# Performance work log

Hardware: AMD Instinct MI355X
Metric: run time of the kernel (lower is better)

## Reference

```python
import jax, jax.numpy as jnp
import numpy as np

B = 128          # batch of codewords
M_CHK = 288      # n_check_nodes
N_VAR = 576      # n_variable_nodes
K_INFO = 288     # n_information_bits
N_ITER = 5
EDGE_P = 0.02    # ~11-12 edges per check row, LDPC-like sparsity


def setup_inputs() -> dict:
    key = jax.random.key(0)
    k1, k2, k3, k4 = jax.random.split(key, 4)
    inputs = jax.random.normal(k1, (B, N_VAR), dtype=jnp.float32)
    # sparse binary parity-check matrix, batched (keras RNN constants carry batch dim)
    H = jax.random.bernoulli(k2, EDGE_P, (B, M_CHK, N_VAR)).astype(jnp.float32)
    sigma2 = 0.5 + 0.5 * jax.random.uniform(k3, (B, 1), dtype=jnp.float32)
    # learned parameters
    input_ponderation = jnp.ones((N_ITER, 1), dtype=jnp.float32)
    out_ponderation = jnp.ones((N_ITER, 1), dtype=jnp.float32)
    skip_ponderation = jnp.ones((1, 1), dtype=jnp.float32)
    # per-edge check-to-variable weights of the neural BP cell
    w_cv = 1.0 + 0.02 * jax.random.normal(k4, (M_CHK, N_VAR), dtype=jnp.float32)
    gate_logit = jnp.asarray(0.0, dtype=jnp.float32)
    return {"inputs": inputs, "H": H, "sigma2": sigma2,
            "input_ponderation": input_ponderation,
            "out_ponderation": out_ponderation,
            "skip_ponderation": skip_ponderation,
            "w_cv": w_cv, "gate_logit": gate_logit}


def _decode(inputs, H, sigma2, input_ponderation, out_ponderation,
            skip_ponderation, w_cv, gate_logit):
    llrs = -4.0 * inputs / sigma2                                    # [B, n]
    # trainable=True path: normalize by mean |llr|
    norm_llrs = llrs / jnp.mean(jnp.abs(llrs), axis=-1, keepdims=True)
    # tile over iterations and apply input ponderation -> [B, T, n]
    x = norm_llrs[:, None, :] * input_ponderation

    mask = H                                                         # [B, m, n]
    gate = jax.nn.sigmoid(gate_logit)

    def cell(Mstate, x_t):
        # variable-to-check extrinsic messages on edges
        S = jnp.sum(Mstate, axis=1, keepdims=True)                   # [B, 1, n]
        V = (x_t[:, None, :] + S - Mstate) * mask                    # [B, m, n]
        # tanh-product check-node update (product excluding self via divide)
        t = jnp.tanh(0.5 * jnp.clip(V, -15.0, 15.0))
        t_edge = jnp.where(mask > 0, t, 1.0)
        P = jnp.prod(t_edge, axis=-1, keepdims=True)                 # [B, m, 1]
        t_safe = jnp.where(jnp.abs(t_edge) < 1e-7,
                           jnp.where(t_edge >= 0, 1e-7, -1e-7), t_edge)
        r = jnp.clip(P / t_safe, -1.0 + 1e-6, 1.0 - 1e-6)
        M_new = 2.0 * jnp.arctanh(r) * w_cv * mask                   # weighted c2v
        # gated (damped) state update
        M_out = gate * M_new + (1.0 - gate) * Mstate
        posterior = x_t + jnp.sum(M_out, axis=1)                     # [B, n]
        return M_out, posterior

    M0 = jnp.zeros_like(H)
    xs = jnp.swapaxes(x, 0, 1)                                       # [T, B, n]
    _, posts = jax.lax.scan(cell, M0, xs)
    outputs = jnp.swapaxes(posts, 0, 1)                              # [B, T, n]

    # post-normalization per iteration, weighted pooling over iterations
    norm_out = outputs / jnp.mean(jnp.abs(outputs), axis=-1, keepdims=True)
    pooled = jnp.mean(out_ponderation * norm_out, axis=-2)           # [B, n]
    out = pooled + skip_ponderation * norm_llrs                      # [1,1] broadcast
    return jax.nn.sigmoid(-out[:, :K_INFO])


def reference(inputs, H, sigma2, input_ponderation, out_ponderation,
              skip_ponderation, w_cv, gate_logit):
    return _decode(inputs, H, sigma2, input_ponderation, out_ponderation,
                   skip_ponderation, w_cv, gate_logit)
```

## Files before the change

### kernel.cpp

```cpp
#include <hip/hip_runtime.h>

#define B_SZ 128
#define MCHK 288
#define NVAR 576
#define KINFO 288
#define NITER 5
#define CAP 40
#define LCAP 3712
#define TPB 1024

__global__ __launch_bounds__(TPB) void decode(
    const float* __restrict__ inp,   const float* __restrict__ H,
    const float* __restrict__ sigma2,
    const float* __restrict__ ipond, const float* __restrict__ opond,
    const float* __restrict__ skipp, const float* __restrict__ wcv,
    const float* __restrict__ gatel, float* __restrict__ out) {

    __shared__ __align__(16) float MT[2 * LCAP];
    __shared__ unsigned int ev[LCAP];
    __shared__ float xln[NVAR];
    __shared__ float S[NVAR];
    __shared__ float pooled[NVAR];
    __shared__ float Prow[MCHK];
    __shared__ int   rcnt[MCHK];
    __shared__ int   roff[MCHK];
    __shared__ float red[16];
    __shared__ int   wsumI[16];
    __shared__ float scal;
    __shared__ int   EtotS;

    float* const Mld = MT;
    float* const tld = MT + LCAP;
    unsigned short* const stage = (unsigned short*)MT;

    const int b    = blockIdx.x;
    const int tid  = threadIdx.x;
    const int wid  = tid >> 6;
    const int lane = tid & 63;

    const float sig  = sigma2[b];
    const float gate = 1.0f / (1.0f + __expf(-gatel[0]));
    const float gbar = 1.0f - gate;
    const float skip = skipp[0];

    float l = 0.0f;
    if (tid < NVAR) l = -4.0f * inp[(size_t)b * NVAR + tid] / sig;

    const float* Hb = H + (size_t)b * (MCHK * NVAR);
    for (int m = wid; m < MCHK; m += 16) {
        const float* hrow = Hb + (size_t)m * NVAR;
        const float4* h4  = (const float4*)hrow;
        float4 a  = h4[lane];
        float4 bq = h4[64 + lane];
        float  c  = hrow[512 + lane];
        int cnt = (a.x!=0.f)+(a.y!=0.f)+(a.z!=0.f)+(a.w!=0.f)
                + (bq.x!=0.f)+(bq.y!=0.f)+(bq.z!=0.f)+(bq.w!=0.f) + (c!=0.f);
        int pre = cnt;
        #pragma unroll
        for (int o = 1; o < 64; o <<= 1) {
            int n = __shfl_up(pre, o, 64);
            if (lane >= o) pre += n;
        }
        int p = pre - cnt;
        unsigned short* dst = stage + m * CAP;
        int base = lane * 4;
        if (a.x!=0.f)  { if (p<CAP) dst[p] = (unsigned short)(base    ); p++; }
        if (a.y!=0.f)  { if (p<CAP) dst[p] = (unsigned short)(base + 1); p++; }
        if (a.z!=0.f)  { if (p<CAP) dst[p] = (unsigned short)(base + 2); p++; }
        if (a.w!=0.f)  { if (p<CAP) dst[p] = (unsigned short)(base + 3); p++; }
        if (bq.x!=0.f) { if (p<CAP) dst[p] = (unsigned short)(256 + base    ); p++; }
        if (bq.y!=0.f) { if (p<CAP) dst[p] = (unsigned short)(256 + base + 1); p++; }
        if (bq.z!=0.f) { if (p<CAP) dst[p] = (unsigned short)(256 + base + 2); p++; }
        if (bq.w!=0.f) { if (p<CAP) dst[p] = (unsigned short)(256 + base + 3); p++; }
        if (c!=0.f)    { if (p<CAP) dst[p] = (unsigned short)(512 + lane);     p++; }
        if (lane == 63) rcnt[m] = (pre > CAP) ? CAP : pre;
    }
    __syncthreads();

    int myc = 0, incl = 0;
    if (tid < 320) {
        myc  = (tid < MCHK) ? rcnt[tid] : 0;
        incl = myc;
        #pragma unroll
        for (int o = 1; o < 64; o <<= 1) {
            int n = __shfl_up(incl, o, 64);
            if (lane >= o) incl += n;
        }
        if (lane == 63) wsumI[wid] = incl;
    }
    __syncthreads();
    if (tid < MCHK) {
        int o = incl - myc;
        #pragma unroll
        for (int w = 0; w < 4; ++w) if (w < wid) o += wsumI[w];
        int c = myc;
        if (o >= LCAP)         { o = 0; c = 0; }
        else if (o + c > LCAP) { c = LCAP - o; }
        roff[tid] = o; rcnt[tid] = c;
        const unsigned short* sg = stage + tid * CAP;
        for (int j = 0; j < c; ++j)
            ev[o + j] = ((unsigned)tid << 16) | (unsigned)sg[j];
    }
    if (tid == 0) {
        int e = wsumI[0] + wsumI[1] + wsumI[2] + wsumI[3] + wsumI[4];
        EtotS = (e > LCAP) ? LCAP : e;
    }
    __syncthreads();
    const int E = EtotS;

    float al = (tid < NVAR) ? fabsf(l) : 0.0f;
    #pragma unroll
    for (int o = 32; o; o >>= 1) al += __shfl_down(al, o, 64);
    if (lane == 0) red[wid] = al;
    for (int e = tid; e < E; e += TPB) Mld[e] = 0.0f;
    if (tid < NVAR) { S[tid] = 0.0f; pooled[tid] = 0.0f; }
    __syncthreads();
    if (tid == 0) {
        float s = 0.0f;
        #pragma unroll
        for (int i = 0; i < 16; ++i) s += red[i];
        scal = (float)NVAR / s;
    }
    __syncthreads();
    if (tid < NVAR) xln[tid] = l * scal;
    __syncthreads();

    float ipl[NITER], opl[NITER];
    #pragma unroll
    for (int t = 0; t < NITER; ++t) { ipl[t] = ipond[t]; opl[t] = opond[t]; }

    for (int t = 0; t < NITER; ++t) {
        const float pt = ipl[t], ot = opl[t];

        for (int e = tid; e < E; e += TPB) {
            int v   = (int)(ev[e] & 0xFFFFu);
            float V = fmaf(pt, xln[v], S[v]) - Mld[e];
            V = fminf(15.0f, fmaxf(-15.0f, V));
            float ex = __expf(V);
            float te = (ex - 1.0f) * __builtin_amdgcn_rcpf(ex + 1.0f);
            float x  = 0.5f * V, x2 = x * x;
            float tp = x * fmaf(x2, fmaf(x2, fmaf(x2, -0.05396825f, 0.13333333f),
                                         -0.33333333f), 1.0f);
            tld[e] = (fabsf(V) < 0.5f) ? tp : te;
        }
        __syncthreads();

        if (tid < MCHK) {
            int c = rcnt[tid], o = roff[tid];
            float P = 1.0f;
            for (int j = 0; j < c; ++j) P *= tld[o + j];
            Prow[tid] = P;
        }
        if (tid < NVAR) S[tid] = 0.0f;
        __syncthreads();

        for (int e = tid; e < E; e += TPB) {
            unsigned pk = ev[e];
            int v = (int)(pk & 0xFFFFu);
            int m = (int)(pk >> 16);
            float tj = tld[e];
            float ts = (fabsf(tj) < 1e-7f) ? ((tj >= 0.0f) ? 1e-7f : -1e-7f) : tj;
            float r  = Prow[m] * __builtin_amdgcn_rcpf(ts);
            r = fminf(1.0f - 1e-6f, fmaxf(-1.0f + 1e-6f, r));
            float w  = wcv[m * NVAR + v];
            float Mn = __logf((1.0f + r) * __builtin_amdgcn_rcpf(1.0f - r)) * w;
            float Mo = fmaf(gate, Mn, gbar * Mld[e]);
            Mld[e] = Mo;
            atomicAdd(&S[v], Mo);
        }
        __syncthreads();

        float post = 0.0f, ap = 0.0f;
        if (tid < NVAR) { post = fmaf(pt, xln[tid], S[tid]); ap = fabsf(post); }
        #pragma unroll
        for (int o = 32; o; o >>= 1) ap += __shfl_down(ap, o, 64);
        if (lane == 0) red[wid] = ap;
        __syncthreads();
        if (tid == 0) {
            float s2 = 0.0f;
            #pragma unroll
            for (int i = 0; i < 16; ++i) s2 += red[i];
            scal = (float)NVAR / s2;
        }
        __syncthreads();
        if (tid < NVAR) pooled[tid] += ot * post * scal;
    }

    if (tid < KINFO) {
        float o = pooled[tid] * (1.0f / NITER) + skip * xln[tid];
        out[(size_t)b * KINFO + tid] = 1.0f / (1.0f + __expf(o));
    }
}

extern "C" void kernel_launch(void* const* d_in, const int* in_sizes, int n_in,
                              void* d_out, int out_size, void* d_ws, size_t ws_size,
                              hipStream_t stream) {
    const float* inp    = (const float*)d_in[0];
    const float* H      = (const float*)d_in[1];
    const float* sigma2 = (const float*)d_in[2];
    const float* ipond  = (const float*)d_in[3];
    const float* opond  = (const float*)d_in[4];
    const float* skipp  = (const float*)d_in[5];
    const float* wcv    = (const float*)d_in[6];
    const float* gatel  = (const float*)d_in[7];
    float* out = (float*)d_out;

    decode<<<B_SZ, TPB, 0, stream>>>(inp, H, sigma2, ipond, opond, skipp,
                                     wcv, gatel, out);
}
```

Baseline: 177.2 us.

## Keep per-edge state in registers, prefetch H rows, drop serial reduction syncs

Per-edge messages, edge indices, edge weights and tanh values now live in registers (up to 4 edges per thread) rather than in LDS, and the w_cv gather is hoisted out of the iteration loop. H row loads are software-prefetched one row-group ahead during edge-list construction. The single-thread scale reductions with their extra barriers are replaced by every thread summing the 16 partials redundantly. This shrinks LDS use and cuts barriers and global gathers, at the cost of more registers and a hard cap of 4096 edges per block, which LCAP already enforces.

```diff
diff --git a/kernel.cpp b/kernel.cpp
--- a/kernel.cpp
+++ b/kernel.cpp
@@ -8,6 +8,7 @@
 #define CAP 40
 #define LCAP 3712
 #define TPB 1024
+#define EPT 4
 
 __global__ __launch_bounds__(TPB) void decode(
     const float* __restrict__ inp,   const float* __restrict__ H,
@@ -16,7 +17,7 @@
     const float* __restrict__ skipp, const float* __restrict__ wcv,
     const float* __restrict__ gatel, float* __restrict__ out) {
 
-    __shared__ __align__(16) float MT[2 * LCAP];
+    __shared__ __align__(16) float MT[(MCHK * CAP) / 2];
     __shared__ unsigned int ev[LCAP];
     __shared__ float xln[NVAR];
     __shared__ float S[NVAR];
@@ -26,11 +27,9 @@
     __shared__ int   roff[MCHK];
     __shared__ float red[16];
     __shared__ int   wsumI[16];
-    __shared__ float scal;
     __shared__ int   EtotS;
 
-    float* const Mld = MT;
-    float* const tld = MT + LCAP;
+    float* const tld = MT;
     unsigned short* const stage = (unsigned short*)MT;
 
     const int b    = blockIdx.x;
@@ -43,37 +42,55 @@
     const float gbar = 1.0f - gate;
     const float skip = skipp[0];
 
+    float ipl[NITER], opl[NITER];
+    #pragma unroll
+    for (int t = 0; t < NITER; ++t) { ipl[t] = ipond[t]; opl[t] = opond[t]; }
+
     float l = 0.0f;
     if (tid < NVAR) l = -4.0f * inp[(size_t)b * NVAR + tid] / sig;
-
-    const float* Hb = H + (size_t)b * (MCHK * NVAR);
-    for (int m = wid; m < MCHK; m += 16) {
-        const float* hrow = Hb + (size_t)m * NVAR;
-        const float4* h4  = (const float4*)hrow;
-        float4 a  = h4[lane];
-        float4 bq = h4[64 + lane];
-        float  c  = hrow[512 + lane];
-        int cnt = (a.x!=0.f)+(a.y!=0.f)+(a.z!=0.f)+(a.w!=0.f)
-                + (bq.x!=0.f)+(bq.y!=0.f)+(bq.z!=0.f)+(bq.w!=0.f) + (c!=0.f);
-        int pre = cnt;
-        #pragma unroll
-        for (int o = 1; o < 64; o <<= 1) {
-            int n = __shfl_up(pre, o, 64);
-            if (lane >= o) pre += n;
-        }
-        int p = pre - cnt;
-        unsigned short* dst = stage + m * CAP;
-        int base = lane * 4;
-        if (a.x!=0.f)  { if (p<CAP) dst[p] = (unsigned short)(base    ); p++; }
-        if (a.y!=0.f)  { if (p<CAP) dst[p] = (unsigned short)(base + 1); p++; }
-        if (a.z!=0.f)  { if (p<CAP) dst[p] = (unsigned short)(base + 2); p++; }
-        if (a.w!=0.f)  { if (p<CAP) dst[p] = (unsigned short)(base + 3); p++; }
-        if (bq.x!=0.f) { if (p<CAP) dst[p] = (unsigned short)(256 + base    ); p++; }
-        if (bq.y!=0.f) { if (p<CAP) dst[p] = (unsigned short)(256 + base + 1); p++; }
-        if (bq.z!=0.f) { if (p<CAP) dst[p] = (unsigned short)(256 + base + 2); p++; }
-        if (bq.w!=0.f) { if (p<CAP) dst[p] = (unsigned short)(256 + base + 3); p++; }
-        if (c!=0.f)    { if (p<CAP) dst[p] = (unsigned short)(512 + lane);     p++; }
-        if (lane == 63) rcnt[m] = (pre > CAP) ? CAP : pre;
+    float al = (tid < NVAR) ? fabsf(l) : 0.0f;
+    #pragma unroll
+    for (int o = 32; o; o >>= 1) al += __shfl_down(al, o, 64);
+    if (lane == 0) red[wid] = al;
+
+    {
+        const float* Hb = H + (size_t)b * (MCHK * NVAR);
+        const float* hr0 = Hb + (size_t)wid * NVAR;
+        float4 a  = ((const float4*)hr0)[lane];
+        float4 bq = ((const float4*)hr0)[64 + lane];
+        float  hc = hr0[512 + lane];
+        for (int m = wid; m < MCHK; m += 16) {
+            const int mn = m + 16;
+            float4 na = a, nbq = bq; float nhc = hc;
+            if (mn < MCHK) {
+                const float* hr = Hb + (size_t)mn * NVAR;
+                na  = ((const float4*)hr)[lane];
+                nbq = ((const float4*)hr)[64 + lane];
+                nhc = hr[512 + lane];
+            }
+            int cnt = (a.x!=0.f)+(a.y!=0.f)+(a.z!=0.f)+(a.w!=0.f)
+                    + (bq.x!=0.f)+(bq.y!=0.f)+(bq.z!=0.f)+(bq.w!=0.f) + (hc!=0.f);
+            int pre = cnt;
+            #pragma unroll
+            for (int o = 1; o < 64; o <<= 1) {
+                int n = __shfl_up(pre, o, 64);
+                if (lane >= o) pre += n;
+            }
+            int p = pre - cnt;
+            unsigned short* dst = stage + m * CAP;
+            int base = lane * 4;
+            if (a.x!=0.f)  { if (p<CAP) dst[p] = (unsigned short)(base    ); p++; }
+            if (a.y!=0.f)  { if (p<CAP) dst[p] = (unsigned short)(base + 1); p++; }
+            if (a.z!=0.f)  { if (p<CAP) dst[p] = (unsigned short)(base + 2); p++; }
+            if (a.w!=0.f)  { if (p<CAP) dst[p] = (unsigned short)(base + 3); p++; }
+            if (bq.x!=0.f) { if (p<CAP) dst[p] = (unsigned short)(256 + base    ); p++; }
+            if (bq.y!=0.f) { if (p<CAP) dst[p] = (unsigned short)(256 + base + 1); p++; }
+            if (bq.z!=0.f) { if (p<CAP) dst[p] = (unsigned short)(256 + base + 2); p++; }
+            if (bq.w!=0.f) { if (p<CAP) dst[p] = (unsigned short)(256 + base + 3); p++; }
+            if (hc!=0.f)   { if (p<CAP) dst[p] = (unsigned short)(512 + lane);     p++; }
+            if (lane == 63) rcnt[m] = (pre > CAP) ? CAP : pre;
+            a = na; bq = nbq; hc = nhc;
+        }
     }
     __syncthreads();
 
@@ -101,6 +118,7 @@
         for (int j = 0; j < c; ++j)
             ev[o + j] = ((unsigned)tid << 16) | (unsigned)sg[j];
     }
+    if (tid < NVAR) { S[tid] = 0.0f; pooled[tid] = 0.0f; }
     if (tid == 0) {
         int e = wsumI[0] + wsumI[1] + wsumI[2] + wsumI[3] + wsumI[4];
         EtotS = (e > LCAP) ? LCAP : e;
@@ -108,65 +126,81 @@
     __syncthreads();
     const int E = EtotS;
 
-    float al = (tid < NVAR) ? fabsf(l) : 0.0f;
+    {
+        float s = 0.0f;
+        #pragma unroll
+        for (int i = 0; i < 16; ++i) s += red[i];
+        const float sc = (float)NVAR / s;
+        if (tid < NVAR) xln[tid] = l * sc;
+    }
+    unsigned evr[EPT]; float wre[EPT], Ml[EPT], tre[EPT];
     #pragma unroll
-    for (int o = 32; o; o >>= 1) al += __shfl_down(al, o, 64);
-    if (lane == 0) red[wid] = al;
-    for (int e = tid; e < E; e += TPB) Mld[e] = 0.0f;
-    if (tid < NVAR) { S[tid] = 0.0f; pooled[tid] = 0.0f; }
-    __syncthreads();
-    if (tid == 0) {
-        float s = 0.0f;
-        #pragma unroll
-        for (int i = 0; i < 16; ++i) s += red[i];
-        scal = (float)NVAR / s;
-    }
-    __syncthreads();
-    if (tid < NVAR) xln[tid] = l * scal;
-    __syncthreads();
-
-    float ipl[NITER], opl[NITER];
-    #pragma unroll
-    for (int t = 0; t < NITER; ++t) { ipl[t] = ipond[t]; opl[t] = opond[t]; }
+    for (int k = 0; k < EPT; ++k) {
+        evr[k] = 0u; wre[k] = 0.0f; Ml[k] = 0.0f; tre[k] = 0.0f;
+        const int e = tid + k * TPB;
+        if (e < E) {
+            const unsigned pk = ev[e];
+            evr[k] = pk;
+            wre[k] = wcv[(pk >> 16) * NVAR + (pk & 0xFFFFu)];
+        }
+    }
+    __syncthreads();
 
     for (int t = 0; t < NITER; ++t) {
         const float pt = ipl[t], ot = opl[t];
 
-        for (int e = tid; e < E; e += TPB) {
-            int v   = (int)(ev[e] & 0xFFFFu);
-            float V = fmaf(pt, xln[v], S[v]) - Mld[e];
-            V = fminf(15.0f, fmaxf(-15.0f, V));
-            float ex = __expf(V);
-            float te = (ex - 1.0f) * __builtin_amdgcn_rcpf(ex + 1.0f);
-            float x  = 0.5f * V, x2 = x * x;
-            float tp = x * fmaf(x2, fmaf(x2, fmaf(x2, -0.05396825f, 0.13333333f),
-                                         -0.33333333f), 1.0f);
-            tld[e] = (fabsf(V) < 0.5f) ? tp : te;
+        #pragma unroll
+        for (int k = 0; k < EPT; ++k) {
+            const int e = tid + k * TPB;
+            if (e < E) {
+                const int v = (int)(evr[k] & 0xFFFFu);
+                float V = fmaf(pt, xln[v], S[v]) - Ml[k];
+                V = fminf(15.0f, fmaxf(-15.0f, V));
+                float ex = __expf(V);
+                float te = (ex - 1.0f) * __builtin_amdgcn_rcpf(ex + 1.0f);
+                float x  = 0.5f * V, x2 = x * x;
+                float tp = x * fmaf(x2, fmaf(x2, fmaf(x2, -0.05396825f, 0.13333333f),
+                                             -0.33333333f), 1.0f);
+                const float tv = (fabsf(V) < 0.5f) ? tp : te;
+                tre[k] = tv;
+                tld[e] = tv;
+            }
         }
         __syncthreads();
 
         if (tid < MCHK) {
-            int c = rcnt[tid], o = roff[tid];
+            const int c = rcnt[tid], o = roff[tid];
             float P = 1.0f;
-            for (int j = 0; j < c; ++j) P *= tld[o + j];
+            if (c > 0) {
+                float cur = tld[o];
+                for (int j = 1; j < c; ++j) {
+                    const float nx = tld[o + j];
+                    P *= cur;
+                    cur = nx;
+                }
+                P *= cur;
+            }
             Prow[tid] = P;
         }
         if (tid < NVAR) S[tid] = 0.0f;
         __syncthreads();
 
-        for (int e = tid; e < E; e += TPB) {
-            unsigned pk = ev[e];
-            int v = (int)(pk & 0xFFFFu);
-            int m = (int)(pk >> 16);
-            float tj = tld[e];
-            float ts = (fabsf(tj) < 1e-7f) ? ((tj >= 0.0f) ? 1e-7f : -1e-7f) : tj;
-            float r  = Prow[m] * __builtin_amdgcn_rcpf(ts);
-            r = fminf(1.0f - 1e-6f, fmaxf(-1.0f + 1e-6f, r));
-            float w  = wcv[m * NVAR + v];
-            float Mn = __logf((1.0f + r) * __builtin_amdgcn_rcpf(1.0f - r)) * w;
-            float Mo = fmaf(gate, Mn, gbar * Mld[e]);
-            Mld[e] = Mo;
-            atomicAdd(&S[v], Mo);
+        #pragma unroll
+        for (int k = 0; k < EPT; ++k) {
+            const int e = tid + k * TPB;
+            if (e < E) {
+                const unsigned pk = evr[k];
+                const int v = (int)(pk & 0xFFFFu);
+                const int m = (int)(pk >> 16);
+                const float tj = tre[k];
+                const float ts = (fabsf(tj) < 1e-7f) ? ((tj >= 0.0f) ? 1e-7f : -1e-7f) : tj;
+                float r = Prow[m] * __builtin_amdgcn_rcpf(ts);
+                r = fminf(1.0f - 1e-6f, fmaxf(-1.0f + 1e-6f, r));
+                const float Mn = __logf((1.0f + r) * __builtin_amdgcn_rcpf(1.0f - r)) * wre[k];
+                const float Mo = fmaf(gate, Mn, gbar * Ml[k]);
+                Ml[k] = Mo;
+                atomicAdd(&S[v], Mo);
+            }
         }
         __syncthreads();
 
@@ -176,14 +210,10 @@
         for (int o = 32; o; o >>= 1) ap += __shfl_down(ap, o, 64);
         if (lane == 0) red[wid] = ap;
         __syncthreads();
-        if (tid == 0) {
-            float s2 = 0.0f;
-            #pragma unroll
-            for (int i = 0; i < 16; ++i) s2 += red[i];
-            scal = (float)NVAR / s2;
-        }
-        __syncthreads();
-        if (tid < NVAR) pooled[tid] += ot * post * scal;
+        float s2 = 0.0f;
+        #pragma unroll
+        for (int i = 0; i < 16; ++i) s2 += red[i];
+        if (tid < NVAR) pooled[tid] += ot * post * ((float)NVAR / s2);
     }
 
     if (tid < KINFO) {
```

Measured after the change: 170.5 us. 3.8% less time.

## Map check rows to wavefronts with register-resident edge state and shuffle products

Applied to the files above, without the earlier changes.

Each wavefront now owns a fixed set of 18 check rows, with one lane per edge, so edge indices, weights and messages stay in registers instead of a compacted LDS edge list. The row product of tanh values is formed with wave shuffles, which removes the separate Prow pass and one barrier per iteration. The S accumulator is double-buffered, and the per-iteration normalisation reductions are deferred to the end, which cuts more barriers. H row loads are software-prefetched one row ahead. The change assumes at most 64 edges per row (CAP 40) and that rows divide evenly across waves.

```diff
diff --git a/kernel.cpp b/kernel.cpp
--- a/kernel.cpp
+++ b/kernel.cpp
@@ -6,32 +6,23 @@
 #define KINFO 288
 #define NITER 5
 #define CAP 40
-#define LCAP 3712
 #define TPB 1024
+#define NWAVES (TPB / 64)
+#define RPW (MCHK / NWAVES)
 
 __global__ __launch_bounds__(TPB) void decode(
-    const float* __restrict__ inp,   const float* __restrict__ H,
-    const float* __restrict__ sigma2,
+    const float* __restrict__ H,
+    const float* __restrict__ inp,   const float* __restrict__ sigma2,
     const float* __restrict__ ipond, const float* __restrict__ opond,
     const float* __restrict__ skipp, const float* __restrict__ wcv,
     const float* __restrict__ gatel, float* __restrict__ out) {
 
-    __shared__ __align__(16) float MT[2 * LCAP];
-    __shared__ unsigned int ev[LCAP];
+    __shared__ unsigned short stage[MCHK * CAP];
     __shared__ float xln[NVAR];
-    __shared__ float S[NVAR];
-    __shared__ float pooled[NVAR];
-    __shared__ float Prow[MCHK];
+    __shared__ float Sb[2][NVAR];
     __shared__ int   rcnt[MCHK];
-    __shared__ int   roff[MCHK];
     __shared__ float red[16];
-    __shared__ int   wsumI[16];
-    __shared__ float scal;
-    __shared__ int   EtotS;
-
-    float* const Mld = MT;
-    float* const tld = MT + LCAP;
-    unsigned short* const stage = (unsigned short*)MT;
+    __shared__ float redT[NITER][16];
 
     const int b    = blockIdx.x;
     const int tid  = threadIdx.x;
@@ -43,151 +34,157 @@
     const float gbar = 1.0f - gate;
     const float skip = skipp[0];
 
+    float ipl[NITER], opl[NITER];
+    #pragma unroll
+    for (int t = 0; t < NITER; ++t) { ipl[t] = ipond[t]; opl[t] = opond[t]; }
+
     float l = 0.0f;
     if (tid < NVAR) l = -4.0f * inp[(size_t)b * NVAR + tid] / sig;
-
-    const float* Hb = H + (size_t)b * (MCHK * NVAR);
-    for (int m = wid; m < MCHK; m += 16) {
-        const float* hrow = Hb + (size_t)m * NVAR;
-        const float4* h4  = (const float4*)hrow;
-        float4 a  = h4[lane];
-        float4 bq = h4[64 + lane];
-        float  c  = hrow[512 + lane];
-        int cnt = (a.x!=0.f)+(a.y!=0.f)+(a.z!=0.f)+(a.w!=0.f)
-                + (bq.x!=0.f)+(bq.y!=0.f)+(bq.z!=0.f)+(bq.w!=0.f) + (c!=0.f);
-        int pre = cnt;
-        #pragma unroll
-        for (int o = 1; o < 64; o <<= 1) {
-            int n = __shfl_up(pre, o, 64);
-            if (lane >= o) pre += n;
-        }
-        int p = pre - cnt;
-        unsigned short* dst = stage + m * CAP;
-        int base = lane * 4;
-        if (a.x!=0.f)  { if (p<CAP) dst[p] = (unsigned short)(base    ); p++; }
-        if (a.y!=0.f)  { if (p<CAP) dst[p] = (unsigned short)(base + 1); p++; }
-        if (a.z!=0.f)  { if (p<CAP) dst[p] = (unsigned short)(base + 2); p++; }
-        if (a.w!=0.f)  { if (p<CAP) dst[p] = (unsigned short)(base + 3); p++; }
-        if (bq.x!=0.f) { if (p<CAP) dst[p] = (unsigned short)(256 + base    ); p++; }
-        if (bq.y!=0.f) { if (p<CAP) dst[p] = (unsigned short)(256 + base + 1); p++; }
-        if (bq.z!=0.f) { if (p<CAP) dst[p] = (unsigned short)(256 + base + 2); p++; }
-        if (bq.w!=0.f) { if (p<CAP) dst[p] = (unsigned short)(256 + base + 3); p++; }
-        if (c!=0.f)    { if (p<CAP) dst[p] = (unsigned short)(512 + lane);     p++; }
-        if (lane == 63) rcnt[m] = (pre > CAP) ? CAP : pre;
-    }
-    __syncthreads();
-
-    int myc = 0, incl = 0;
-    if (tid < 320) {
-        myc  = (tid < MCHK) ? rcnt[tid] : 0;
-        incl = myc;
-        #pragma unroll
-        for (int o = 1; o < 64; o <<= 1) {
-            int n = __shfl_up(incl, o, 64);
-            if (lane >= o) incl += n;
-        }
-        if (lane == 63) wsumI[wid] = incl;
-    }
-    __syncthreads();
-    if (tid < MCHK) {
-        int o = incl - myc;
-        #pragma unroll
-        for (int w = 0; w < 4; ++w) if (w < wid) o += wsumI[w];
-        int c = myc;
-        if (o >= LCAP)         { o = 0; c = 0; }
-        else if (o + c > LCAP) { c = LCAP - o; }
-        roff[tid] = o; rcnt[tid] = c;
-        const unsigned short* sg = stage + tid * CAP;
-        for (int j = 0; j < c; ++j)
-            ev[o + j] = ((unsigned)tid << 16) | (unsigned)sg[j];
-    }
-    if (tid == 0) {
-        int e = wsumI[0] + wsumI[1] + wsumI[2] + wsumI[3] + wsumI[4];
-        EtotS = (e > LCAP) ? LCAP : e;
-    }
-    __syncthreads();
-    const int E = EtotS;
-
     float al = (tid < NVAR) ? fabsf(l) : 0.0f;
     #pragma unroll
     for (int o = 32; o; o >>= 1) al += __shfl_down(al, o, 64);
     if (lane == 0) red[wid] = al;
-    for (int e = tid; e < E; e += TPB) Mld[e] = 0.0f;
-    if (tid < NVAR) { S[tid] = 0.0f; pooled[tid] = 0.0f; }
+
+    {
+        const float* Hb = H + (size_t)b * (MCHK * NVAR);
+        const int m0 = wid * RPW;
+        const float* hr = Hb + (size_t)m0 * NVAR;
+        float4 a = ((const float4*)hr)[lane];
+        float4 q = ((const float4*)hr)[64 + lane];
+        float  c = hr[512 + lane];
+        #pragma unroll
+        for (int i = 0; i < RPW; ++i) {
+            const int m = m0 + i;
+            float4 na = a, nq = q; float nc = c;
+            if (i < RPW - 1) {
+                const float* hn = Hb + (size_t)(m + 1) * NVAR;
+                na = ((const float4*)hn)[lane];
+                nq = ((const float4*)hn)[64 + lane];
+                nc = hn[512 + lane];
+            }
+            int cnt = (a.x!=0.f)+(a.y!=0.f)+(a.z!=0.f)+(a.w!=0.f)
+                    + (q.x!=0.f)+(q.y!=0.f)+(q.z!=0.f)+(q.w!=0.f) + (c!=0.f);
+            int pre = cnt;
+            #pragma unroll
+            for (int o = 1; o < 64; o <<= 1) {
+                int n = __shfl_up(pre, o, 64);
+                if (lane >= o) pre += n;
+            }
+            int p = pre - cnt;
+            unsigned short* dst = stage + m * CAP;
+            int base = lane * 4;
+            if (a.x!=0.f) { if (p<CAP) dst[p] = (unsigned short)(base    ); p++; }
+            if (a.y!=0.f) { if (p<CAP) dst[p] = (unsigned short)(base + 1); p++; }
+            if (a.z!=0.f) { if (p<CAP) dst[p] = (unsigned short)(base + 2); p++; }
+            if (a.w!=0.f) { if (p<CAP) dst[p] = (unsigned short)(base + 3); p++; }
+            if (q.x!=0.f) { if (p<CAP) dst[p] = (unsigned short)(256 + base    ); p++; }
+            if (q.y!=0.f) { if (p<CAP) dst[p] = (unsigned short)(256 + base + 1); p++; }
+            if (q.z!=0.f) { if (p<CAP) dst[p] = (unsigned short)(256 + base + 2); p++; }
+            if (q.w!=0.f) { if (p<CAP) dst[p] = (unsigned short)(256 + base + 3); p++; }
+            if (c!=0.f)   { if (p<CAP) dst[p] = (unsigned short)(512 + lane);     p++; }
+            if (lane == 63) rcnt[m] = (pre > CAP) ? CAP : pre;
+            a = na; q = nq; c = nc;
+        }
+    }
     __syncthreads();
-    if (tid == 0) {
+
+    {
         float s = 0.0f;
         #pragma unroll
         for (int i = 0; i < 16; ++i) s += red[i];
-        scal = (float)NVAR / s;
+        const float sc = (float)NVAR / s;
+        if (tid < NVAR) {
+            xln[tid]   = l * sc;
+            Sb[0][tid] = 0.0f;
+            Sb[1][tid] = 0.0f;
+        }
+    }
+
+    int   vr[RPW];  float wr[RPW], Ml[RPW];  int cntr[RPW];
+    #pragma unroll
+    for (int r2 = 0; r2 < RPW; ++r2) {
+        const int m = wid * RPW + r2;
+        const int c = rcnt[m];
+        cntr[r2] = c;
+        int v = 0; float w = 0.0f;
+        if (lane < c) {
+            v = stage[m * CAP + lane];
+            w = wcv[m * NVAR + v];
+        }
+        vr[r2] = v; wr[r2] = w; Ml[r2] = 0.0f;
     }
     __syncthreads();
-    if (tid < NVAR) xln[tid] = l * scal;
-    __syncthreads();
-
-    float ipl[NITER], opl[NITER];
-    #pragma unroll
-    for (int t = 0; t < NITER; ++t) { ipl[t] = ipond[t]; opl[t] = opond[t]; }
-
+
+    float p[NITER];
+    #pragma unroll
+    for (int t = 0; t < NITER; ++t) p[t] = 0.0f;
+
+    #pragma unroll
     for (int t = 0; t < NITER; ++t) {
-        const float pt = ipl[t], ot = opl[t];
-
-        for (int e = tid; e < E; e += TPB) {
-            int v   = (int)(ev[e] & 0xFFFFu);
-            float V = fmaf(pt, xln[v], S[v]) - Mld[e];
+        const float pt = ipl[t];
+        float* const sr = Sb[t & 1];
+        float* const sa = Sb[(t + 1) & 1];
+
+        #pragma unroll
+        for (int r2 = 0; r2 < RPW; ++r2) {
+            const bool act = (lane < cntr[r2]);
+            const int  v   = vr[r2];
+            float V = 0.0f;
+            if (act) V = fmaf(pt, xln[v], sr[v]) - Ml[r2];
             V = fminf(15.0f, fmaxf(-15.0f, V));
             float ex = __expf(V);
             float te = (ex - 1.0f) * __builtin_amdgcn_rcpf(ex + 1.0f);
             float x  = 0.5f * V, x2 = x * x;
             float tp = x * fmaf(x2, fmaf(x2, fmaf(x2, -0.05396825f, 0.13333333f),
                                          -0.33333333f), 1.0f);
-            tld[e] = (fabsf(V) < 0.5f) ? tp : te;
+            const float tv = (fabsf(V) < 0.5f) ? tp : te;
+            float P = act ? tv : 1.0f;
+            P *= __shfl_xor(P,  1, 64);
+            P *= __shfl_xor(P,  2, 64);
+            P *= __shfl_xor(P,  4, 64);
+            P *= __shfl_xor(P,  8, 64);
+            P *= __shfl_xor(P, 16, 64);
+            P *= __shfl_xor(P, 32, 64);
+            if (act) {
+                const float ts = (fabsf(tv) < 1e-7f)
+                               ? ((tv >= 0.0f) ? 1e-7f : -1e-7f) : tv;
+                float r = P * __builtin_amdgcn_rcpf(ts);
+                r = fminf(1.0f - 1e-6f, fmaxf(-1.0f + 1e-6f, r));
+                const float Mn = __logf((1.0f + r) * __builtin_amdgcn_rcpf(1.0f - r))
+                               * wr[r2];
+                const float Mo = fmaf(gate, Mn, gbar * Ml[r2]);
+                Ml[r2] = Mo;
+                atomicAdd(&sa[v], Mo);
+            }
         }
         __syncthreads();
 
-        if (tid < MCHK) {
-            int c = rcnt[tid], o = roff[tid];
-            float P = 1.0f;
-            for (int j = 0; j < c; ++j) P *= tld[o + j];
-            Prow[tid] = P;
-        }
-        if (tid < NVAR) S[tid] = 0.0f;
+        if (tid < NVAR) {
+            p[t] = fmaf(pt, xln[tid], sa[tid]);
+            sr[tid] = 0.0f;
+        }
         __syncthreads();
-
-        for (int e = tid; e < E; e += TPB) {
-            unsigned pk = ev[e];
-            int v = (int)(pk & 0xFFFFu);
-            int m = (int)(pk >> 16);
-            float tj = tld[e];
-            float ts = (fabsf(tj) < 1e-7f) ? ((tj >= 0.0f) ? 1e-7f : -1e-7f) : tj;
-            float r  = Prow[m] * __builtin_amdgcn_rcpf(ts);
-            r = fminf(1.0f - 1e-6f, fmaxf(-1.0f + 1e-6f, r));
-            float w  = wcv[m * NVAR + v];
-            float Mn = __logf((1.0f + r) * __builtin_amdgcn_rcpf(1.0f - r)) * w;
-            float Mo = fmaf(gate, Mn, gbar * Mld[e]);
-            Mld[e] = Mo;
-            atomicAdd(&S[v], Mo);
-        }
-        __syncthreads();
-
-        float post = 0.0f, ap = 0.0f;
-        if (tid < NVAR) { post = fmaf(pt, xln[tid], S[tid]); ap = fabsf(post); }
+    }
+
+    #pragma unroll
+    for (int t = 0; t < NITER; ++t) {
+        float ap = (tid < NVAR) ? fabsf(p[t]) : 0.0f;
         #pragma unroll
         for (int o = 32; o; o >>= 1) ap += __shfl_down(ap, o, 64);
-        if (lane == 0) red[wid] = ap;
-        __syncthreads();
-        if (tid == 0) {
+        if (lane == 0) redT[t][wid] = ap;
+    }
+    __syncthreads();
+
+    if (tid < KINFO) {
+        float pooled = 0.0f;
+        #pragma unroll
+        for (int t = 0; t < NITER; ++t) {
             float s2 = 0.0f;
             #pragma unroll
-            for (int i = 0; i < 16; ++i) s2 += red[i];
-            scal = (float)NVAR / s2;
-        }
-        __syncthreads();
-        if (tid < NVAR) pooled[tid] += ot * post * scal;
-    }
-
-    if (tid < KINFO) {
-        float o = pooled[tid] * (1.0f / NITER) + skip * xln[tid];
+            for (int i = 0; i < 16; ++i) s2 += redT[t][i];
+            pooled += opl[t] * p[t] * ((float)NVAR / s2);
+        }
+        float o = pooled * (1.0f / NITER) + skip * xln[tid];
         out[(size_t)b * KINFO + tid] = 1.0f / (1.0f + __expf(o));
     }
 }
@@ -205,6 +202,6 @@
     const float* gatel  = (const float*)d_in[7];
     float* out = (float*)d_out;
 
-    decode<<<B_SZ, TPB, 0, stream>>>(inp, H, sigma2, ipond, opond, skipp,
+    decode<<<B_SZ, TPB, 0, stream>>>(H, inp, sigma2, ipond, opond, skipp,
                                      wcv, gatel, out);
 }
```

New measurement: 193.8 us. 1.09x slower.
